# Kernel tuning notes

Measured on AMD Instinct MI355X. Metric: run time of the kernel, lower is better.

Reference implementation:

```python
import jax, jax.numpy as jnp
import numpy as np
from jax import lax


def _binarize(t):
    # sign binarization to +1/-1 (zero maps to -1, matching torch.where(t > 0, 1, -1))
    return jnp.where(t > 0, 1.0, -1.0).astype(t.dtype)


def _bconv(x, w, b):
    # binary conv: binarize input and weights, then standard 3x3 'same' conv
    y = lax.conv_general_dilated(
        _binarize(x), _binarize(w),
        window_strides=(1, 1), padding=((1, 1), (1, 1)),
        dimension_numbers=('NCHW', 'OIHW', 'NCHW'))
    return y + b[None, :, None, None]


def _maxpool2(x):
    return lax.reduce_window(x, -jnp.inf, lax.max, (1, 1, 2, 2), (1, 1, 2, 2), 'VALID')


def setup_inputs() -> dict:
    key = jax.random.key(0)
    ks = jax.random.split(key, 13)
    s = 0.1
    return {
        'x': jax.random.normal(ks[0], (4096, 1, 28, 28), jnp.float32),
        'w1': jax.random.normal(ks[1], (32, 1, 3, 3), jnp.float32) * s,
        'b1': jax.random.normal(ks[2], (32,), jnp.float32) * s,
        'w2': jax.random.normal(ks[3], (64, 32, 3, 3), jnp.float32) * s,
        'b2': jax.random.normal(ks[4], (64,), jnp.float32) * s,
        'w3': jax.random.normal(ks[5], (16, 64, 3, 3), jnp.float32) * s,
        'b3': jax.random.normal(ks[6], (16,), jnp.float32) * s,
        'fc1_w': jax.random.normal(ks[7], (256, 16 * 7 * 7), jnp.float32) * s,
        'fc1_b': jax.random.normal(ks[8], (256,), jnp.float32) * s,
        'fc2_w': jax.random.normal(ks[9], (128, 256), jnp.float32) * s,
        'fc2_b': jax.random.normal(ks[10], (128,), jnp.float32) * s,
        'fc3_w': jax.random.normal(ks[11], (10, 128), jnp.float32) * s,
        'fc3_b': jax.random.normal(ks[12], (10,), jnp.float32) * s,
    }


def reference(x, w1, b1, w2, b2, w3, b3, fc1_w, fc1_b, fc2_w, fc2_b, fc3_w, fc3_b):
    h = jax.nn.relu(_maxpool2(_bconv(x, w1, b1)))      # [B,32,14,14]
    h = jax.nn.relu(_maxpool2(_bconv(h, w2, b2)))      # [B,64,7,7]
    h = jax.nn.relu(_bconv(h, w3, b3))                 # [B,16,7,7]
    h = h.reshape(-1, 16 * 7 * 7)
    h = jax.nn.relu(h @ fc1_w.T + fc1_b)
    h = jax.nn.relu(h @ fc2_w.T + fc2_b)
    return h @ fc3_w.T + fc3_b                          # [B,10]
```

## Files before the change

### kernel.cpp

```cpp
#include <hip/hip_runtime.h>
#include <cstdint>

#define OFF_PW    0
#define OFF_W1T   4096
#define OFF_W2T   823296
#define OFF_H3T   954368
#define OFF_H1T   14061568
#define OFF_H2T   18255872

__global__ __launch_bounds__(256) void prep(
    const float* __restrict__ w1, const float* __restrict__ w2,
    const float* __restrict__ w3,
    const float* __restrict__ fc1_w, const float* __restrict__ fc2_w,
    uint32_t* __restrict__ pw, float* __restrict__ w1T, float* __restrict__ w2T) {
    int t = threadIdx.x;
    if (blockIdx.x == 0) {
        if (t < 32) {
            uint32_t b = 0;
            for (int k = 0; k < 9; ++k) b |= (w1[t * 9 + k] > 0.f ? 1u : 0u) << k;
            pw[t] = b;
        }
        for (int idx = t; idx < 576; idx += 256) {
            int oc = idx / 9, tap = idx % 9;
            int kh = tap / 3, kw = tap % 3;
            uint32_t b = 0;
            for (int ic = 0; ic < 32; ++ic)
                b |= (w2[((oc * 32 + ic) * 3 + kh) * 3 + kw] > 0.f ? 1u : 0u) << ic;
            pw[32 + idx] = b;
        }
        for (int idx = t; idx < 144; idx += 256) {
            int oc = idx / 9, tap = idx % 9;
            int kh = tap / 3, kw = tap % 3;
            uint32_t lo = 0, hi = 0;
            for (int ic = 0; ic < 32; ++ic) {
                lo |= (w3[((oc * 64 + ic) * 3 + kh) * 3 + kw] > 0.f ? 1u : 0u) << ic;
                hi |= (w3[((oc * 64 + ic + 32) * 3 + kh) * 3 + kw] > 0.f ? 1u : 0u) << ic;
            }
            pw[608 + idx * 2] = lo;
            pw[608 + idx * 2 + 1] = hi;
        }
    } else {
        int e = (blockIdx.x - 1) * 256 + t;
        if (e < 204800) {
            int k = e >> 8, n = e & 255;
            w1T[e] = (k < 784) ? fc1_w[n * 784 + k] : 0.f;
        } else {
            int e2 = e - 204800;
            int k = e2 >> 7, n = e2 & 127;
            w2T[e2] = fc2_w[n * 256 + k];
        }
    }
}

__global__ __launch_bounds__(256) void conv_stack(
    const float* __restrict__ x,
    const float* __restrict__ b1, const float* __restrict__ b2,
    const float* __restrict__ b3,
    const uint32_t* __restrict__ pw,
    float* __restrict__ h3T) {
    __shared__ uint32_t s_wb1[32];
    __shared__ uint32_t s_W2[576];
    __shared__ uint32_t s_W3[288];
    __shared__ float s_b1[32], s_b2[64], s_b3[16];
    __shared__ uint32_t s_xrow[28];
    __shared__ uint32_t s_H1[256];
    __shared__ uint32_t s_H2[162];

    const int t = threadIdx.x;
    const int img = blockIdx.x;

    s_H1[t] = 0;
    if (t < 162) s_H2[t] = 0;
    if (t < 32) { s_wb1[t] = pw[t]; s_b1[t] = b1[t]; }
    if (t >= 32 && t < 96) s_b2[t - 32] = b2[t - 32];
    if (t >= 96 && t < 112) s_b3[t - 96] = b3[t - 96];
    for (int i = t; i < 576; i += 256) s_W2[i] = pw[32 + i];
    for (int i = t; i < 288; i += 256) s_W3[i] = pw[608 + i];
    if (t >= 192 && t < 220) {
        int r = t - 192;
        const float* xr = x + img * 784 + r * 28;
        uint32_t b = 0;
        for (int j = 0; j < 28; ++j) b |= (xr[j] > 0.f ? 1u : 0u) << j;
        s_xrow[r] = b;
    }
    __syncthreads();

    if (t < 196) {
        int pi = t / 14, pj = t % 14;
        uint32_t sarr[4], marr[4];
        int pcm[4];
#pragma unroll
        for (int p = 0; p < 4; ++p) {
            int i = 2 * pi + (p >> 1), j = 2 * pj + (p & 1);
            uint32_t sb = 0, mb = 0;
            int bit = 0;
#pragma unroll
            for (int di = -1; di <= 1; ++di) {
                int y = i + di;
                bool rv = (unsigned)y < 28u;
                uint32_t row = rv ? s_xrow[rv ? y : 0] : 0u;
#pragma unroll
                for (int dj = -1; dj <= 1; ++dj) {
                    int xx = j + dj;
                    bool v = rv && (unsigned)xx < 28u;
                    if (v) {
                        mb |= 1u << bit;
                        sb |= ((row >> xx) & 1u) << bit;
                    }
                    ++bit;
                }
            }
            sarr[p] = sb; marr[p] = mb; pcm[p] = __popc(mb);
        }
        uint32_t word = 0;
#pragma unroll
        for (int c = 0; c < 32; ++c) {
            uint32_t w = s_wb1[c];
            int best = -1000;
#pragma unroll
            for (int p = 0; p < 4; ++p) {
                int v = pcm[p] - 2 * __popc((sarr[p] ^ w) & marr[p]);
                best = v > best ? v : best;
            }
            word |= ((float)best + s_b1[c] > 0.f ? 1u : 0u) << c;
        }
        s_H1[(pi + 1) * 16 + (pj + 1)] = word;
    }
    __syncthreads();

    for (int task = t; task < 400; task += 256) {
        int q = task / 25, ip = task - q * 25;
        int pi = ip / 5 + 1, pj = ip % 5 + 1;
        uint32_t cell[16];
#pragma unroll
        for (int r = 0; r < 4; ++r)
#pragma unroll
            for (int c = 0; c < 4; ++c)
                cell[r * 4 + c] = s_H1[(2 * pi + r) * 16 + (2 * pj + c)];
        uint32_t nib = 0;
#pragma unroll
        for (int o = 0; o < 4; ++o) {
            int oc = q * 4 + o;
            const uint32_t* wrow = &s_W2[oc * 9];
            int best = -100000;
#pragma unroll
            for (int a = 0; a < 2; ++a)
#pragma unroll
                for (int b = 0; b < 2; ++b) {
                    int S = 0;
#pragma unroll
                    for (int kh = 0; kh < 3; ++kh)
#pragma unroll
                        for (int kw = 0; kw < 3; ++kw)
                            S += __popc(cell[(a + kh) * 4 + (b + kw)] ^ wrow[kh * 3 + kw]);
                    int v = 288 - 2 * S;
                    best = v > best ? v : best;
                }
            nib |= ((float)best + s_b2[oc] > 0.f ? 1u : 0u) << (oc & 31);
        }
        atomicOr((unsigned int*)&s_H2[((pi + 1) * 9 + (pj + 1)) * 2 + (q >> 3)],
                 (unsigned int)nib);
    }
    for (int task = t; task < 384; task += 256) {
        int q = task / 24, bp = task - q * 24;
        int pi, pj;
        if (bp < 7)       { pi = 0; pj = bp; }
        else if (bp < 14) { pi = 6; pj = bp - 7; }
        else if (bp < 19) { pi = bp - 13; pj = 0; }
        else              { pi = bp - 18; pj = 6; }
        uint32_t vr[4], vc[4];
#pragma unroll
        for (int r = 0; r < 4; ++r) {
            vr[r] = ((unsigned)(2 * pi - 1 + r) < 14u) ? 0xFFFFFFFFu : 0u;
            vc[r] = ((unsigned)(2 * pj - 1 + r) < 14u) ? 0xFFFFFFFFu : 0u;
        }
        uint32_t cell[16], V[16];
#pragma unroll
        for (int r = 0; r < 4; ++r)
#pragma unroll
            for (int c = 0; c < 4; ++c) {
                cell[r * 4 + c] = s_H1[(2 * pi + r) * 16 + (2 * pj + c)];
                V[r * 4 + c] = vr[r] & vc[c];
            }
        int nvp[4];
#pragma unroll
        for (int a = 0; a < 2; ++a)
#pragma unroll
            for (int b = 0; b < 2; ++b) {
                int i = 2 * pi + a, j = 2 * pj + b;
                int vy = 3 - (i == 0) - (i == 13);
                int vx = 3 - (j == 0) - (j == 13);
                nvp[a * 2 + b] = 32 * vy * vx;
            }
        uint32_t nib = 0;
#pragma unroll
        for (int o = 0; o < 4; ++o) {
            int oc = q * 4 + o;
            const uint32_t* wrow = &s_W2[oc * 9];
            int best = -100000;
#pragma unroll
            for (int a = 0; a < 2; ++a)
#pragma unroll
                for (int b = 0; b < 2; ++b) {
                    int S = 0;
#pragma unroll
                    for (int kh = 0; kh < 3; ++kh)
#pragma unroll
                        for (int kw = 0; kw < 3; ++kw) {
                            int ci = (a + kh) * 4 + (b + kw);
                            S += __popc((cell[ci] ^ wrow[kh * 3 + kw]) & V[ci]);
                        }
                    int v = nvp[a * 2 + b] - 2 * S;
                    best = v > best ? v : best;
                }
            nib |= ((float)best + s_b2[oc] > 0.f ? 1u : 0u) << (oc & 31);
        }
        atomicOr((unsigned int*)&s_H2[((pi + 1) * 9 + (pj + 1)) * 2 + (q >> 3)],
                 (unsigned int)nib);
    }
    __syncthreads();

    for (int task = t; task < 784; task += 256) {
        int oc = task / 49, pos = task - oc * 49;
        int pi = pos / 7, pj = pos % 7;
        uint32_t vr[3], vc[3];
#pragma unroll
        for (int d = 0; d < 3; ++d) {
            vr[d] = ((unsigned)(pi - 1 + d) < 7u) ? 0xFFFFFFFFu : 0u;
            vc[d] = ((unsigned)(pj - 1 + d) < 7u) ? 0xFFFFFFFFu : 0u;
        }
        int vy = 3 - (pi == 0) - (pi == 6);
        int vx = 3 - (pj == 0) - (pj == 6);
        int Nv = 64 * vy * vx;
        const uint32_t* wr = &s_W3[oc * 18];
        int S = 0;
#pragma unroll
        for (int kh = 0; kh < 3; ++kh)
#pragma unroll
            for (int kw = 0; kw < 3; ++kw) {
                uint32_t V = vr[kh] & vc[kw];
                int idx = ((pi + kh) * 9 + (pj + kw)) * 2;
                S += __popc((s_H2[idx] ^ wr[(kh * 3 + kw) * 2]) & V);
                S += __popc((s_H2[idx + 1] ^ wr[(kh * 3 + kw) * 2 + 1]) & V);
            }
        float h = (float)(Nv - 2 * S) + s_b3[oc];
        h3T[task * 4096 + img] = h > 0.f ? h : 0.f;
    }
}

__global__ __launch_bounds__(256) void fc1_gemm(
    const float* __restrict__ aT,
    const float* __restrict__ bT,
    const float* __restrict__ bias,
    float* __restrict__ oT) {
    const int KC = 80, LD = 68;
    __shared__ float As[KC * LD];
    __shared__ float Bs[KC * LD];
    const int t = threadIdx.x;
    const int tx = t & 15, ty = t >> 4;
    const int img0 = blockIdx.x * 64;
    const int n0 = blockIdx.y * 64;
    float acc[4][4] = {{0.f}};

    for (int kc = 0; kc < 800; kc += KC) {
#pragma unroll
        for (int s = 0; s < 5; ++s) {
            int v = t + s * 256;
            int kk = v >> 4, i4 = (v & 15) * 4;
            *(float4*)&As[kk * LD + i4] =
                *(const float4*)&aT[(kc + kk) * 4096 + img0 + i4];
            *(float4*)&Bs[kk * LD + i4] =
                *(const float4*)&bT[(kc + kk) * 256 + n0 + i4];
        }
        __syncthreads();
#pragma unroll 4
        for (int kk = 0; kk < KC; ++kk) {
            float4 a = *(const float4*)&As[kk * LD + ty * 4];
            float4 b = *(const float4*)&Bs[kk * LD + tx * 4];
            acc[0][0] += a.x * b.x; acc[0][1] += a.x * b.y;
            acc[0][2] += a.x * b.z; acc[0][3] += a.x * b.w;
            acc[1][0] += a.y * b.x; acc[1][1] += a.y * b.y;
            acc[1][2] += a.y * b.z; acc[1][3] += a.y * b.w;
            acc[2][0] += a.z * b.x; acc[2][1] += a.z * b.y;
            acc[2][2] += a.z * b.z; acc[2][3] += a.z * b.w;
            acc[3][0] += a.w * b.x; acc[3][1] += a.w * b.y;
            acc[3][2] += a.w * b.z; acc[3][3] += a.w * b.w;
        }
        __syncthreads();
    }
    float4 bb = *(const float4*)&bias[n0 + tx * 4];
    float bv[4] = {bb.x, bb.y, bb.z, bb.w};
#pragma unroll
    for (int jj = 0; jj < 4; ++jj) {
        float4 ov;
        ov.x = acc[0][jj] + bv[jj]; ov.x = ov.x > 0.f ? ov.x : 0.f;
        ov.y = acc[1][jj] + bv[jj]; ov.y = ov.y > 0.f ? ov.y : 0.f;
        ov.z = acc[2][jj] + bv[jj]; ov.z = ov.z > 0.f ? ov.z : 0.f;
        ov.w = acc[3][jj] + bv[jj]; ov.w = ov.w > 0.f ? ov.w : 0.f;
        *(float4*)&oT[(n0 + tx * 4 + jj) * 4096 + img0 + ty * 4] = ov;
    }
}

__global__ __launch_bounds__(256) void fc2_gemm(
    const float* __restrict__ aT,
    const float* __restrict__ bT,
    const float* __restrict__ bias,
    float* __restrict__ oT) {
    const int KC = 64, LDA = 68, LDB = 36;
    __shared__ float As[KC * LDA];
    __shared__ float Bs[KC * LDB];
    const int t = threadIdx.x;
    const int tx = t & 15, ty = t >> 4;
    const int img0 = blockIdx.x * 64;
    const int n0 = blockIdx.y * 32;
    float acc[4][2] = {{0.f}};

    for (int kc = 0; kc < 256; kc += KC) {
#pragma unroll
        for (int s = 0; s < 4; ++s) {
            int v = t + s * 256;
            int kk = v >> 4, i4 = (v & 15) * 4;
            *(float4*)&As[kk * LDA + i4] =
                *(const float4*)&aT[(kc + kk) * 4096 + img0 + i4];
        }
#pragma unroll
        for (int s = 0; s < 2; ++s) {
            int v = t + s * 256;
            int kk = v >> 3, n4 = (v & 7) * 4;
            *(float4*)&Bs[kk * LDB + n4] =
                *(const float4*)&bT[(kc + kk) * 128 + n0 + n4];
        }
        __syncthreads();
#pragma unroll 4
        for (int kk = 0; kk < KC; ++kk) {
            float4 a = *(const float4*)&As[kk * LDA + ty * 4];
            float2 b = *(const float2*)&Bs[kk * LDB + tx * 2];
            acc[0][0] += a.x * b.x; acc[0][1] += a.x * b.y;
            acc[1][0] += a.y * b.x; acc[1][1] += a.y * b.y;
            acc[2][0] += a.z * b.x; acc[2][1] += a.z * b.y;
            acc[3][0] += a.w * b.x; acc[3][1] += a.w * b.y;
        }
        __syncthreads();
    }
#pragma unroll
    for (int j = 0; j < 2; ++j) {
        int n = n0 + tx * 2 + j;
        float bj = bias[n];
        float4 ov;
        ov.x = acc[0][j] + bj; ov.x = ov.x > 0.f ? ov.x : 0.f;
        ov.y = acc[1][j] + bj; ov.y = ov.y > 0.f ? ov.y : 0.f;
        ov.z = acc[2][j] + bj; ov.z = ov.z > 0.f ? ov.z : 0.f;
        ov.w = acc[3][j] + bj; ov.w = ov.w > 0.f ? ov.w : 0.f;
        *(float4*)&oT[n * 4096 + img0 + ty * 4] = ov;
    }
}

__global__ __launch_bounds__(256) void fc3_gemm(
    const float* __restrict__ aT,
    const float* __restrict__ w,
    const float* __restrict__ bias,
    float* __restrict__ out) {
    int id = blockIdx.x * 256 + threadIdx.x;
    int n = id >> 12, img = id & 4095;
    const float* wr = w + n * 128;
    float a0 = 0.f, a1 = 0.f, a2 = 0.f, a3 = 0.f;
#pragma unroll 8
    for (int k = 0; k < 128; k += 4) {
        a0 += aT[(k + 0) * 4096 + img] * wr[k + 0];
        a1 += aT[(k + 1) * 4096 + img] * wr[k + 1];
        a2 += aT[(k + 2) * 4096 + img] * wr[k + 2];
        a3 += aT[(k + 3) * 4096 + img] * wr[k + 3];
    }
    out[img * 10 + n] = (a0 + a1) + (a2 + a3) + bias[n];
}

extern "C" void kernel_launch(void* const* d_in, const int* in_sizes, int n_in,
                              void* d_out, int out_size, void* d_ws, size_t ws_size,
                              hipStream_t stream) {
    const float* x     = (const float*)d_in[0];
    const float* w1    = (const float*)d_in[1];
    const float* b1    = (const float*)d_in[2];
    const float* w2    = (const float*)d_in[3];
    const float* b2    = (const float*)d_in[4];
    const float* w3    = (const float*)d_in[5];
    const float* b3    = (const float*)d_in[6];
    const float* fc1_w = (const float*)d_in[7];
    const float* fc1_b = (const float*)d_in[8];
    const float* fc2_w = (const float*)d_in[9];
    const float* fc2_b = (const float*)d_in[10];
    const float* fc3_w = (const float*)d_in[11];
    const float* fc3_b = (const float*)d_in[12];
    float* out = (float*)d_out;

    const int B = in_sizes[0] / 784;
    char* ws = (char*)d_ws;
    uint32_t* pw = (uint32_t*)(ws + OFF_PW);
    float* w1T = (float*)(ws + OFF_W1T);
    float* w2T = (float*)(ws + OFF_W2T);
    float* h3T = (float*)(ws + OFF_H3T);
    float* h1T = (float*)(ws + OFF_H1T);
    float* h2T = (float*)(ws + OFF_H2T);

    hipLaunchKernelGGL(prep, dim3(929), dim3(256), 0, stream,
                       w1, w2, w3, fc1_w, fc2_w, pw, w1T, w2T);
    hipLaunchKernelGGL(conv_stack, dim3(B), dim3(256), 0, stream,
                       x, b1, b2, b3, pw, h3T);
    hipLaunchKernelGGL(fc1_gemm, dim3(B / 64, 4), dim3(256), 0, stream,
                       h3T, w1T, fc1_b, h1T);
    hipLaunchKernelGGL(fc2_gemm, dim3(B / 64, 4), dim3(256), 0, stream,
                       h1T, w2T, fc2_b, h2T);
    hipLaunchKernelGGL(fc3_gemm, dim3(B * 10 / 256), dim3(256), 0, stream,
                       h2T, fc3_w, fc3_b, out);
}
```

Before: 220.1 us.

## Rework binary conv stack with border corrections and double-buffered FC GEMMs

Rewrites the weight prep as a flat per-element kernel that packs sign bits with atomicOr, and zero-fills the padded rows of the fc1 activation buffer. The conv kernel now uses unmasked popcounts for interior pixels and precomputed border-correction tables for edges, compares against integer thresholds instead of float bias adds, and splits conv2/conv3 work by output-channel groups across threads. The fc1 and fc2 GEMMs gain register-staged double buffering in shared memory. These target ALU work in the conv stack and load latency in the GEMMs, at the cost of more complex indexing and an extra memset launch.

Result: slower. 250.5 us (+13.8%).

```diff
diff --git a/kernel.cpp b/kernel.cpp
--- a/kernel.cpp
+++ b/kernel.cpp
@@ -12,57 +12,64 @@
     const float* __restrict__ w1, const float* __restrict__ w2,
     const float* __restrict__ w3,
     const float* __restrict__ fc1_w, const float* __restrict__ fc2_w,
-    uint32_t* __restrict__ pw, float* __restrict__ w1T, float* __restrict__ w2T) {
-    int t = threadIdx.x;
-    if (blockIdx.x == 0) {
-        if (t < 32) {
-            uint32_t b = 0;
-            for (int k = 0; k < 9; ++k) b |= (w1[t * 9 + k] > 0.f ? 1u : 0u) << k;
-            pw[t] = b;
-        }
-        for (int idx = t; idx < 576; idx += 256) {
-            int oc = idx / 9, tap = idx % 9;
-            int kh = tap / 3, kw = tap % 3;
-            uint32_t b = 0;
-            for (int ic = 0; ic < 32; ++ic)
-                b |= (w2[((oc * 32 + ic) * 3 + kh) * 3 + kw] > 0.f ? 1u : 0u) << ic;
-            pw[32 + idx] = b;
-        }
-        for (int idx = t; idx < 144; idx += 256) {
-            int oc = idx / 9, tap = idx % 9;
-            int kh = tap / 3, kw = tap % 3;
-            uint32_t lo = 0, hi = 0;
-            for (int ic = 0; ic < 32; ++ic) {
-                lo |= (w3[((oc * 64 + ic) * 3 + kh) * 3 + kw] > 0.f ? 1u : 0u) << ic;
-                hi |= (w3[((oc * 64 + ic + 32) * 3 + kh) * 3 + kw] > 0.f ? 1u : 0u) << ic;
-            }
-            pw[608 + idx * 2] = lo;
-            pw[608 + idx * 2 + 1] = hi;
-        }
-    } else {
-        int e = (blockIdx.x - 1) * 256 + t;
-        if (e < 204800) {
-            int k = e >> 8, n = e & 255;
-            w1T[e] = (k < 784) ? fc1_w[n * 784 + k] : 0.f;
-        } else {
-            int e2 = e - 204800;
-            int k = e2 >> 7, n = e2 & 127;
-            w2T[e2] = fc2_w[n * 256 + k];
-        }
-    }
-}
-
-__global__ __launch_bounds__(256) void conv_stack(
-    const float* __restrict__ x,
-    const float* __restrict__ b1, const float* __restrict__ b2,
-    const float* __restrict__ b3,
-    const uint32_t* __restrict__ pw,
-    float* __restrict__ h3T) {
-    __shared__ uint32_t s_wb1[32];
-    __shared__ uint32_t s_W2[576];
+    uint32_t* __restrict__ pw, float* __restrict__ w1T,
+    float* __restrict__ w2T, float* __restrict__ h3T) {
+    int idx = blockIdx.x * 256 + threadIdx.x;
+    if (idx < 204800) {
+        int k = idx >> 8, n = idx & 255;
+        w1T[idx] = (k < 784) ? fc1_w[n * 784 + k] : 0.f;
+        return;
+    }
+    idx -= 204800;
+    if (idx < 32768) {
+        int k = idx >> 7, n = idx & 127;
+        w2T[idx] = fc2_w[n * 256 + k];
+        return;
+    }
+    idx -= 32768;
+    if (idx < 65536) {
+        h3T[784 * 4096 + idx] = 0.f;
+        return;
+    }
+    idx -= 65536;
+    if (idx < 288) {
+        int c = idx / 9, tap = idx - c * 9;
+        if (w1[idx] > 0.f) atomicOr(&pw[c], 1u << tap);
+        return;
+    }
+    idx -= 288;
+    if (idx < 18432) {
+        int oc = idx / 288, r = idx - oc * 288;
+        int ic = r / 9, tap = r - ic * 9;
+        if (w2[idx] > 0.f) atomicOr(&pw[32 + oc * 9 + tap], 1u << ic);
+        return;
+    }
+    idx -= 18432;
+    if (idx < 9216) {
+        int oc = idx / 576, r = idx - oc * 576;
+        int ic = r / 9, tap = r - ic * 9;
+        if (w3[idx] > 0.f)
+            atomicOr(&pw[608 + oc * 18 + tap * 2 + (ic >> 5)], 1u << (ic & 31));
+    }
+}
+
+__device__ __forceinline__ uint32_t bfe3(uint32_t r, int j) {
+    return (r >> j) & 7u;
+}
+
+__global__ __launch_bounds__(256, 4) void conv_stack(
+    const float* __restrict__ x, const float* __restrict__ b1,
+    const float* __restrict__ b2, const float* __restrict__ b3,
+    const uint32_t* __restrict__ pw, float* __restrict__ h3T) {
+    __shared__ uint32_t s_w1[32];
+    __shared__ int s_ic1[32];
+    __shared__ int s_ic2[64];
+    __shared__ uint32_t s_c2[128];
+    __shared__ uint32_t s_c3[32];
+    __shared__ uint32_t s_W2p[768];
     __shared__ uint32_t s_W3[288];
-    __shared__ float s_b1[32], s_b2[64], s_b3[16];
-    __shared__ uint32_t s_xrow[28];
+    __shared__ float s_b3[16];
+    __shared__ uint32_t s_xr[28];
     __shared__ uint32_t s_H1[256];
     __shared__ uint32_t s_H2[162];
 
@@ -71,212 +78,300 @@
 
     s_H1[t] = 0;
     if (t < 162) s_H2[t] = 0;
-    if (t < 32) { s_wb1[t] = pw[t]; s_b1[t] = b1[t]; }
-    if (t >= 32 && t < 96) s_b2[t - 32] = b2[t - 32];
-    if (t >= 96 && t < 112) s_b3[t - 96] = b3[t - 96];
-    for (int i = t; i < 576; i += 256) s_W2[i] = pw[32 + i];
+    if (t < 28) {
+        const float4* xr = (const float4*)(x + img * 784 + t * 28);
+        uint32_t b = 0;
+#pragma unroll
+        for (int q = 0; q < 7; ++q) {
+            float4 v = xr[q];
+            b |= (v.x > 0.f ? 1u : 0u) << (q * 4 + 0);
+            b |= (v.y > 0.f ? 1u : 0u) << (q * 4 + 1);
+            b |= (v.z > 0.f ? 1u : 0u) << (q * 4 + 2);
+            b |= (v.w > 0.f ? 1u : 0u) << (q * 4 + 3);
+        }
+        s_xr[t] = b << 1;
+    }
+    if (t >= 32 && t < 64) {
+        int c = t - 32;
+        s_w1[c] = pw[c];
+        s_ic1[c] = (int)floorf(-b1[c]) + 1;
+    }
+    if (t >= 64 && t < 128) {
+        int oc = t - 64;
+        s_ic2[oc] = (int)floorf(-b2[oc]) + 1;
+        int p[9];
+#pragma unroll
+        for (int k = 0; k < 9; ++k) p[k] = __popc(pw[32 + oc * 9 + k]);
+        s_c2[oc * 2] = (uint32_t)(p[0] + p[1] + p[2]) |
+                       ((uint32_t)(p[6] + p[7] + p[8]) << 8) |
+                       ((uint32_t)(p[0] + p[3] + p[6]) << 16) |
+                       ((uint32_t)(p[2] + p[5] + p[8]) << 24);
+        s_c2[oc * 2 + 1] = (uint32_t)p[0] | ((uint32_t)p[2] << 8) |
+                           ((uint32_t)p[6] << 16) | ((uint32_t)p[8] << 24);
+    }
+    if (t >= 128 && t < 144) {
+        int oc = t - 128;
+        s_b3[oc] = b3[oc];
+        int p[9];
+#pragma unroll
+        for (int k = 0; k < 9; ++k)
+            p[k] = __popc(pw[608 + oc * 18 + k * 2]) +
+                   __popc(pw[608 + oc * 18 + k * 2 + 1]);
+        s_c3[oc * 2] = (uint32_t)(p[0] + p[1] + p[2]) |
+                       ((uint32_t)(p[6] + p[7] + p[8]) << 8) |
+                       ((uint32_t)(p[0] + p[3] + p[6]) << 16) |
+                       ((uint32_t)(p[2] + p[5] + p[8]) << 24);
+        s_c3[oc * 2 + 1] = (uint32_t)p[0] | ((uint32_t)p[2] << 8) |
+                           ((uint32_t)p[6] << 16) | ((uint32_t)p[8] << 24);
+    }
+    for (int i = t; i < 768; i += 256) {
+        int oc = i / 12, tap = i - oc * 12;
+        s_W2p[i] = (tap < 9) ? pw[32 + oc * 9 + tap] : 0u;
+    }
     for (int i = t; i < 288; i += 256) s_W3[i] = pw[608 + i];
-    if (t >= 192 && t < 220) {
-        int r = t - 192;
-        const float* xr = x + img * 784 + r * 28;
-        uint32_t b = 0;
-        for (int j = 0; j < 28; ++j) b |= (xr[j] > 0.f ? 1u : 0u) << j;
-        s_xrow[r] = b;
-    }
     __syncthreads();
 
     if (t < 196) {
-        int pi = t / 14, pj = t % 14;
-        uint32_t sarr[4], marr[4];
-        int pcm[4];
-#pragma unroll
-        for (int p = 0; p < 4; ++p) {
-            int i = 2 * pi + (p >> 1), j = 2 * pj + (p & 1);
-            uint32_t sb = 0, mb = 0;
-            int bit = 0;
-#pragma unroll
-            for (int di = -1; di <= 1; ++di) {
-                int y = i + di;
-                bool rv = (unsigned)y < 28u;
-                uint32_t row = rv ? s_xrow[rv ? y : 0] : 0u;
-#pragma unroll
-                for (int dj = -1; dj <= 1; ++dj) {
-                    int xx = j + dj;
-                    bool v = rv && (unsigned)xx < 28u;
-                    if (v) {
-                        mb |= 1u << bit;
-                        sb |= ((row >> xx) & 1u) << bit;
-                    }
-                    ++bit;
+        int pi, pj;
+        if (t < 144) { pi = 1 + t / 12; pj = 1 + t % 12; }
+        else {
+            int b = t - 144;
+            if (b < 14)      { pi = 0;  pj = b; }
+            else if (b < 28) { pi = 13; pj = b - 14; }
+            else if (b < 40) { pi = 1 + (b - 28); pj = 0; }
+            else             { pi = 1 + (b - 40); pj = 13; }
+        }
+        uint32_t r[4];
+#pragma unroll
+        for (int k = 0; k < 4; ++k) {
+            int y = 2 * pi - 1 + k;
+            r[k] = ((unsigned)y < 28u) ? s_xr[y] : 0u;
+        }
+        uint32_t samp[4];
+#pragma unroll
+        for (int a = 0; a < 2; ++a)
+#pragma unroll
+            for (int bb = 0; bb < 2; ++bb) {
+                int j = 2 * pj + bb;
+                samp[a * 2 + bb] = bfe3(r[a], j) | (bfe3(r[a + 1], j) << 3) |
+                                   (bfe3(r[a + 2], j) << 6);
+            }
+        uint32_t word = 0;
+        if (t < 144) {
+#pragma unroll 4
+            for (int c = 0; c < 32; ++c) {
+                uint32_t w = s_w1[c];
+                int S = __popc(samp[0] ^ w);
+                int S1 = __popc(samp[1] ^ w); S = S1 < S ? S1 : S;
+                int S2 = __popc(samp[2] ^ w); S = S2 < S ? S2 : S;
+                int S3 = __popc(samp[3] ^ w); S = S3 < S ? S3 : S;
+                word |= (uint32_t)(9 - 2 * S >= s_ic1[c]) << c;
+            }
+        } else {
+            uint32_t inv[4];
+            int Nv[4];
+#pragma unroll
+            for (int a = 0; a < 2; ++a)
+#pragma unroll
+                for (int bb = 0; bb < 2; ++bb) {
+                    int i = 2 * pi + a, j = 2 * pj + bb;
+                    inv[a * 2 + bb] =
+                        (i == 0 ? 0x7u : 0u) | (i == 27 ? 0x1C0u : 0u) |
+                        (j == 0 ? 0x49u : 0u) | (j == 27 ? 0x124u : 0u);
                 }
-            }
-            sarr[p] = sb; marr[p] = mb; pcm[p] = __popc(mb);
-        }
-        uint32_t word = 0;
-#pragma unroll
-        for (int c = 0; c < 32; ++c) {
-            uint32_t w = s_wb1[c];
-            int best = -1000;
-#pragma unroll
-            for (int p = 0; p < 4; ++p) {
-                int v = pcm[p] - 2 * __popc((sarr[p] ^ w) & marr[p]);
-                best = v > best ? v : best;
-            }
-            word |= ((float)best + s_b1[c] > 0.f ? 1u : 0u) << c;
-        }
-        s_H1[(pi + 1) * 16 + (pj + 1)] = word;
+#pragma unroll
+            for (int p = 0; p < 4; ++p) Nv[p] = 9 - __popc(inv[p]);
+#pragma unroll 4
+            for (int c = 0; c < 32; ++c) {
+                uint32_t w = s_w1[c];
+                int vmax = -100;
+#pragma unroll
+                for (int p = 0; p < 4; ++p) {
+                    int v = Nv[p] - 2 * (__popc(samp[p] ^ w) - __popc(w & inv[p]));
+                    vmax = v > vmax ? v : vmax;
+                }
+                word |= (uint32_t)(vmax >= s_ic1[c]) << c;
+            }
+        }
+        s_H1[(pi + 1) * 16 + pj + 1] = word;
     }
     __syncthreads();
 
-    for (int task = t; task < 400; task += 256) {
-        int q = task / 25, ip = task - q * 25;
-        int pi = ip / 5 + 1, pj = ip % 5 + 1;
+    if (t < 245) {
+        int pos = t / 5, grp = t - pos * 5;
+        int pi, pj;
+        if (pos < 25) { pi = 1 + pos / 5; pj = 1 + pos % 5; }
+        else {
+            int b = pos - 25;
+            if (b < 7)       { pi = 0; pj = b; }
+            else if (b < 14) { pi = 6; pj = b - 7; }
+            else if (b < 19) { pi = b - 13; pj = 0; }
+            else             { pi = b - 18; pj = 6; }
+        }
         uint32_t cell[16];
 #pragma unroll
         for (int r = 0; r < 4; ++r)
 #pragma unroll
             for (int c = 0; c < 4; ++c)
                 cell[r * 4 + c] = s_H1[(2 * pi + r) * 16 + (2 * pj + c)];
-        uint32_t nib = 0;
+        const bool border = pos >= 25;
+        int rsh = (pi == 6) ? 8 : 0;
+        uint32_t mR = (pi == 0) ? 0x3u : ((pi == 6) ? 0xCu : 0u);
+        int csh = (pj == 6) ? 24 : 16;
+        uint32_t mC = (pj == 0) ? 0x5u : ((pj == 6) ? 0xAu : 0u);
+        int pcell = ((pi == 6) ? 2 : 0) + ((pj == 6) ? 1 : 0);
+        int psh = pcell * 8;
+        uint32_t mP = (mR && mC) ? (1u << pcell) : 0u;
+        int Nv[4];
+#pragma unroll
+        for (int p = 0; p < 4; ++p) {
+            int rP = (mR >> p) & 1, cP = (mC >> p) & 1;
+            Nv[p] = 32 * (9 - 3 * rP - 3 * cP + (rP & cP));
+        }
+        int ocs = grp * 13;
+        int cnt = (grp < 4) ? 13 : 12;
+        uint32_t lo = 0, hi = 0;
+        for (int oi = 0; oi < cnt; ++oi) {
+            int oc = ocs + oi;
+            const uint32_t* wp = &s_W2p[oc * 12];
+            uint4 wA = *(const uint4*)wp;
+            uint4 wB = *(const uint4*)(wp + 4);
+            uint32_t w8 = wp[8];
+            uint32_t w[9] = {wA.x, wA.y, wA.z, wA.w, wB.x, wB.y, wB.z, wB.w, w8};
+            int S[4];
+#pragma unroll
+            for (int a = 0; a < 2; ++a)
+#pragma unroll
+                for (int bb = 0; bb < 2; ++bb) {
+                    int acc = 0;
+#pragma unroll
+                    for (int kh = 0; kh < 3; ++kh)
+#pragma unroll
+                        for (int kw = 0; kw < 3; ++kw)
+                            acc += __popc(cell[(a + kh) * 4 + (bb + kw)] ^ w[kh * 3 + kw]);
+                    S[a * 2 + bb] = acc;
+                }
+            int bitv;
+            if (!border) {
+                int Sm = S[0];
+                Sm = S[1] < Sm ? S[1] : Sm;
+                Sm = S[2] < Sm ? S[2] : Sm;
+                Sm = S[3] < Sm ? S[3] : Sm;
+                bitv = (288 - 2 * Sm >= s_ic2[oc]) ? 1 : 0;
+            } else {
+                uint32_t cw0 = s_c2[oc * 2], cw1 = s_c2[oc * 2 + 1];
+                int rB = (cw0 >> rsh) & 0xFF;
+                int cB = (cw0 >> csh) & 0xFF;
+                int pB = (cw1 >> psh) & 0xFF;
+                int vmax = -100000;
+#pragma unroll
+                for (int p = 0; p < 4; ++p) {
+                    int corr = (((mR >> p) & 1) ? rB : 0) +
+                               (((mC >> p) & 1) ? cB : 0) -
+                               (((mP >> p) & 1) ? pB : 0);
+                    int v = Nv[p] - 2 * (S[p] - corr);
+                    vmax = v > vmax ? v : vmax;
+                }
+                bitv = (vmax >= s_ic2[oc]) ? 1 : 0;
+            }
+            if (oc < 32) lo |= (uint32_t)bitv << oc;
+            else         hi |= (uint32_t)bitv << (oc - 32);
+        }
+        int hidx = ((pi + 1) * 9 + pj + 1) * 2;
+        if (lo) atomicOr(&s_H2[hidx], lo);
+        if (hi) atomicOr(&s_H2[hidx + 1], hi);
+    }
+    __syncthreads();
+
+    if (t < 196) {
+        int pos = t >> 2, grp = t & 3;
+        int pi, pj;
+        if (pos < 25) { pi = 1 + pos / 5; pj = 1 + pos % 5; }
+        else {
+            int b = pos - 25;
+            if (b < 7)       { pi = 0; pj = b; }
+            else if (b < 14) { pi = 6; pj = b - 7; }
+            else if (b < 19) { pi = b - 13; pj = 0; }
+            else             { pi = b - 18; pj = 6; }
+        }
+        uint32_t cc[18];
+#pragma unroll
+        for (int kh = 0; kh < 3; ++kh)
+#pragma unroll
+            for (int kw = 0; kw < 3; ++kw) {
+                int bidx = ((pi + kh) * 9 + pj + kw) * 2;
+                cc[(kh * 3 + kw) * 2] = s_H2[bidx];
+                cc[(kh * 3 + kw) * 2 + 1] = s_H2[bidx + 1];
+            }
+        const bool border = pos >= 25;
+        int rowAny = (pi == 0) | (pi == 6);
+        int colAny = (pj == 0) | (pj == 6);
+        int rsh = (pi == 6) ? 8 : 0;
+        int csh = (pj == 6) ? 24 : 16;
+        int psh = (((pi == 6) ? 2 : 0) + ((pj == 6) ? 1 : 0)) * 8;
+        int nInv = 3 * rowAny + 3 * colAny - (rowAny & colAny);
+        int NvB = 64 * (9 - nInv);
 #pragma unroll
         for (int o = 0; o < 4; ++o) {
-            int oc = q * 4 + o;
-            const uint32_t* wrow = &s_W2[oc * 9];
-            int best = -100000;
-#pragma unroll
-            for (int a = 0; a < 2; ++a)
-#pragma unroll
-                for (int b = 0; b < 2; ++b) {
-                    int S = 0;
-#pragma unroll
-                    for (int kh = 0; kh < 3; ++kh)
-#pragma unroll
-                        for (int kw = 0; kw < 3; ++kw)
-                            S += __popc(cell[(a + kh) * 4 + (b + kw)] ^ wrow[kh * 3 + kw]);
-                    int v = 288 - 2 * S;
-                    best = v > best ? v : best;
-                }
-            nib |= ((float)best + s_b2[oc] > 0.f ? 1u : 0u) << (oc & 31);
-        }
-        atomicOr((unsigned int*)&s_H2[((pi + 1) * 9 + (pj + 1)) * 2 + (q >> 3)],
-                 (unsigned int)nib);
-    }
-    for (int task = t; task < 384; task += 256) {
-        int q = task / 24, bp = task - q * 24;
-        int pi, pj;
-        if (bp < 7)       { pi = 0; pj = bp; }
-        else if (bp < 14) { pi = 6; pj = bp - 7; }
-        else if (bp < 19) { pi = bp - 13; pj = 0; }
-        else              { pi = bp - 18; pj = 6; }
-        uint32_t vr[4], vc[4];
-#pragma unroll
-        for (int r = 0; r < 4; ++r) {
-            vr[r] = ((unsigned)(2 * pi - 1 + r) < 14u) ? 0xFFFFFFFFu : 0u;
-            vc[r] = ((unsigned)(2 * pj - 1 + r) < 14u) ? 0xFFFFFFFFu : 0u;
-        }
-        uint32_t cell[16], V[16];
-#pragma unroll
-        for (int r = 0; r < 4; ++r)
-#pragma unroll
-            for (int c = 0; c < 4; ++c) {
-                cell[r * 4 + c] = s_H1[(2 * pi + r) * 16 + (2 * pj + c)];
-                V[r * 4 + c] = vr[r] & vc[c];
-            }
-        int nvp[4];
-#pragma unroll
-        for (int a = 0; a < 2; ++a)
-#pragma unroll
-            for (int b = 0; b < 2; ++b) {
-                int i = 2 * pi + a, j = 2 * pj + b;
-                int vy = 3 - (i == 0) - (i == 13);
-                int vx = 3 - (j == 0) - (j == 13);
-                nvp[a * 2 + b] = 32 * vy * vx;
-            }
-        uint32_t nib = 0;
-#pragma unroll
-        for (int o = 0; o < 4; ++o) {
-            int oc = q * 4 + o;
-            const uint32_t* wrow = &s_W2[oc * 9];
-            int best = -100000;
-#pragma unroll
-            for (int a = 0; a < 2; ++a)
-#pragma unroll
-                for (int b = 0; b < 2; ++b) {
-                    int S = 0;
-#pragma unroll
-                    for (int kh = 0; kh < 3; ++kh)
-#pragma unroll
-                        for (int kw = 0; kw < 3; ++kw) {
-                            int ci = (a + kh) * 4 + (b + kw);
-                            S += __popc((cell[ci] ^ wrow[kh * 3 + kw]) & V[ci]);
-                        }
-                    int v = nvp[a * 2 + b] - 2 * S;
-                    best = v > best ? v : best;
-                }
-            nib |= ((float)best + s_b2[oc] > 0.f ? 1u : 0u) << (oc & 31);
-        }
-        atomicOr((unsigned int*)&s_H2[((pi + 1) * 9 + (pj + 1)) * 2 + (q >> 3)],
-                 (unsigned int)nib);
-    }
-    __syncthreads();
-
-    for (int task = t; task < 784; task += 256) {
-        int oc = task / 49, pos = task - oc * 49;
-        int pi = pos / 7, pj = pos % 7;
-        uint32_t vr[3], vc[3];
-#pragma unroll
-        for (int d = 0; d < 3; ++d) {
-            vr[d] = ((unsigned)(pi - 1 + d) < 7u) ? 0xFFFFFFFFu : 0u;
-            vc[d] = ((unsigned)(pj - 1 + d) < 7u) ? 0xFFFFFFFFu : 0u;
-        }
-        int vy = 3 - (pi == 0) - (pi == 6);
-        int vx = 3 - (pj == 0) - (pj == 6);
-        int Nv = 64 * vy * vx;
-        const uint32_t* wr = &s_W3[oc * 18];
-        int S = 0;
-#pragma unroll
-        for (int kh = 0; kh < 3; ++kh)
-#pragma unroll
-            for (int kw = 0; kw < 3; ++kw) {
-                uint32_t V = vr[kh] & vc[kw];
-                int idx = ((pi + kh) * 9 + (pj + kw)) * 2;
-                S += __popc((s_H2[idx] ^ wr[(kh * 3 + kw) * 2]) & V);
-                S += __popc((s_H2[idx + 1] ^ wr[(kh * 3 + kw) * 2 + 1]) & V);
-            }
-        float h = (float)(Nv - 2 * S) + s_b3[oc];
-        h3T[task * 4096 + img] = h > 0.f ? h : 0.f;
-    }
-}
-
-__global__ __launch_bounds__(256) void fc1_gemm(
-    const float* __restrict__ aT,
-    const float* __restrict__ bT,
-    const float* __restrict__ bias,
-    float* __restrict__ oT) {
-    const int KC = 80, LD = 68;
-    __shared__ float As[KC * LD];
-    __shared__ float Bs[KC * LD];
+            int oc = grp * 4 + o;
+            const uint32_t* wp = &s_W3[oc * 18];
+            int S = 0;
+#pragma unroll
+            for (int k = 0; k < 18; ++k) S += __popc(cc[k] ^ wp[k]);
+            int corr = 0;
+            if (border) {
+                uint32_t cw0 = s_c3[oc * 2], cw1 = s_c3[oc * 2 + 1];
+                corr = (rowAny ? (int)((cw0 >> rsh) & 0xFF) : 0) +
+                       (colAny ? (int)((cw0 >> csh) & 0xFF) : 0) -
+                       ((rowAny & colAny) ? (int)((cw1 >> psh) & 0xFF) : 0);
+            }
+            int v = NvB - 2 * (S - corr);
+            float h = (float)v + s_b3[oc];
+            h3T[(oc * 49 + pi * 7 + pj) * 4096 + img] = fmaxf(h, 0.f);
+        }
+    }
+}
+
+__global__ __launch_bounds__(256, 1) void fc1_gemm(
+    const float* __restrict__ aT, const float* __restrict__ bT,
+    const float* __restrict__ bias, float* __restrict__ oT) {
+    __shared__ float As[2][50 * 68];
+    __shared__ float Bs[2][50 * 68];
     const int t = threadIdx.x;
     const int tx = t & 15, ty = t >> 4;
     const int img0 = blockIdx.x * 64;
     const int n0 = blockIdx.y * 64;
     float acc[4][4] = {{0.f}};
 
-    for (int kc = 0; kc < 800; kc += KC) {
-#pragma unroll
-        for (int s = 0; s < 5; ++s) {
-            int v = t + s * 256;
+#pragma unroll
+    for (int s = 0; s < 4; ++s) {
+        int v = t + s * 256;
+        if (v < 800) {
             int kk = v >> 4, i4 = (v & 15) * 4;
-            *(float4*)&As[kk * LD + i4] =
-                *(const float4*)&aT[(kc + kk) * 4096 + img0 + i4];
-            *(float4*)&Bs[kk * LD + i4] =
-                *(const float4*)&bT[(kc + kk) * 256 + n0 + i4];
-        }
-        __syncthreads();
-#pragma unroll 4
-        for (int kk = 0; kk < KC; ++kk) {
-            float4 a = *(const float4*)&As[kk * LD + ty * 4];
-            float4 b = *(const float4*)&Bs[kk * LD + tx * 4];
+            *(float4*)&As[0][kk * 68 + i4] = *(const float4*)&aT[kk * 4096 + img0 + i4];
+            *(float4*)&Bs[0][kk * 68 + i4] = *(const float4*)&bT[kk * 256 + n0 + i4];
+        }
+    }
+    __syncthreads();
+    int cur = 0;
+    for (int ch = 0; ch < 16; ++ch) {
+        float4 ra[4], rb[4];
+        if (ch < 15) {
+            int kc = (ch + 1) * 50;
+#pragma unroll
+            for (int s = 0; s < 4; ++s) {
+                int v = t + s * 256;
+                if (v < 800) {
+                    int kk = v >> 4, i4 = (v & 15) * 4;
+                    ra[s] = *(const float4*)&aT[(kc + kk) * 4096 + img0 + i4];
+                    rb[s] = *(const float4*)&bT[(kc + kk) * 256 + n0 + i4];
+                }
+            }
+        }
+#pragma unroll 5
+        for (int kk = 0; kk < 50; ++kk) {
+            float4 a = *(const float4*)&As[cur][kk * 68 + ty * 4];
+            float4 b = *(const float4*)&Bs[cur][kk * 68 + tx * 4];
             acc[0][0] += a.x * b.x; acc[0][1] += a.x * b.y;
             acc[0][2] += a.x * b.z; acc[0][3] += a.x * b.w;
             acc[1][0] += a.y * b.x; acc[1][1] += a.y * b.y;
@@ -286,7 +381,19 @@
             acc[3][0] += a.w * b.x; acc[3][1] += a.w * b.y;
             acc[3][2] += a.w * b.z; acc[3][3] += a.w * b.w;
         }
+        if (ch < 15) {
+#pragma unroll
+            for (int s = 0; s < 4; ++s) {
+                int v = t + s * 256;
+                if (v < 800) {
+                    int kk = v >> 4, i4 = (v & 15) * 4;
+                    *(float4*)&As[cur ^ 1][kk * 68 + i4] = ra[s];
+                    *(float4*)&Bs[cur ^ 1][kk * 68 + i4] = rb[s];
+                }
+            }
+        }
         __syncthreads();
+        cur ^= 1;
     }
     float4 bb = *(const float4*)&bias[n0 + tx * 4];
     float bv[4] = {bb.x, bb.y, bb.z, bb.w};
@@ -301,46 +408,73 @@
     }
 }
 
-__global__ __launch_bounds__(256) void fc2_gemm(
-    const float* __restrict__ aT,
-    const float* __restrict__ bT,
-    const float* __restrict__ bias,
-    float* __restrict__ oT) {
-    const int KC = 64, LDA = 68, LDB = 36;
-    __shared__ float As[KC * LDA];
-    __shared__ float Bs[KC * LDB];
+__global__ __launch_bounds__(256, 1) void fc2_gemm(
+    const float* __restrict__ aT, const float* __restrict__ bT,
+    const float* __restrict__ bias, float* __restrict__ oT) {
+    __shared__ float As[2][64 * 68];
+    __shared__ float Bs[2][64 * 36];
     const int t = threadIdx.x;
     const int tx = t & 15, ty = t >> 4;
     const int img0 = blockIdx.x * 64;
     const int n0 = blockIdx.y * 32;
     float acc[4][2] = {{0.f}};
 
-    for (int kc = 0; kc < 256; kc += KC) {
-#pragma unroll
-        for (int s = 0; s < 4; ++s) {
-            int v = t + s * 256;
-            int kk = v >> 4, i4 = (v & 15) * 4;
-            *(float4*)&As[kk * LDA + i4] =
-                *(const float4*)&aT[(kc + kk) * 4096 + img0 + i4];
-        }
-#pragma unroll
-        for (int s = 0; s < 2; ++s) {
-            int v = t + s * 256;
-            int kk = v >> 3, n4 = (v & 7) * 4;
-            *(float4*)&Bs[kk * LDB + n4] =
-                *(const float4*)&bT[(kc + kk) * 128 + n0 + n4];
-        }
-        __syncthreads();
+#pragma unroll
+    for (int s = 0; s < 4; ++s) {
+        int v = t + s * 256;
+        int kk = v >> 4, i4 = (v & 15) * 4;
+        *(float4*)&As[0][kk * 68 + i4] = *(const float4*)&aT[kk * 4096 + img0 + i4];
+    }
+#pragma unroll
+    for (int s = 0; s < 2; ++s) {
+        int v = t + s * 256;
+        int kk = v >> 3, n4 = (v & 7) * 4;
+        *(float4*)&Bs[0][kk * 36 + n4] = *(const float4*)&bT[kk * 128 + n0 + n4];
+    }
+    __syncthreads();
+    int cur = 0;
+    for (int ch = 0; ch < 4; ++ch) {
+        float4 ra[4]; float4 rb[2];
+        if (ch < 3) {
+            int kc = (ch + 1) * 64;
+#pragma unroll
+            for (int s = 0; s < 4; ++s) {
+                int v = t + s * 256;
+                int kk = v >> 4, i4 = (v & 15) * 4;
+                ra[s] = *(const float4*)&aT[(kc + kk) * 4096 + img0 + i4];
+            }
+#pragma unroll
+            for (int s = 0; s < 2; ++s) {
+                int v = t + s * 256;
+                int kk = v >> 3, n4 = (v & 7) * 4;
+                rb[s] = *(const float4*)&bT[(kc + kk) * 128 + n0 + n4];
+            }
+        }
 #pragma unroll 4
-        for (int kk = 0; kk < KC; ++kk) {
-            float4 a = *(const float4*)&As[kk * LDA + ty * 4];
-            float2 b = *(const float2*)&Bs[kk * LDB + tx * 2];
+        for (int kk = 0; kk < 64; ++kk) {
+            float4 a = *(const float4*)&As[cur][kk * 68 + ty * 4];
+            float2 b = *(const float2*)&Bs[cur][kk * 36 + tx * 2];
             acc[0][0] += a.x * b.x; acc[0][1] += a.x * b.y;
             acc[1][0] += a.y * b.x; acc[1][1] += a.y * b.y;
             acc[2][0] += a.z * b.x; acc[2][1] += a.z * b.y;
             acc[3][0] += a.w * b.x; acc[3][1] += a.w * b.y;
         }
+        if (ch < 3) {
+#pragma unroll
+            for (int s = 0; s < 4; ++s) {
+                int v = t + s * 256;
+                int kk = v >> 4, i4 = (v & 15) * 4;
+                *(float4*)&As[cur ^ 1][kk * 68 + i4] = ra[s];
+            }
+#pragma unroll
+            for (int s = 0; s < 2; ++s) {
+                int v = t + s * 256;
+                int kk = v >> 3, n4 = (v & 7) * 4;
+                *(float4*)&Bs[cur ^ 1][kk * 36 + n4] = rb[s];
+            }
+        }
         __syncthreads();
+        cur ^= 1;
     }
 #pragma unroll
     for (int j = 0; j < 2; ++j) {
@@ -356,10 +490,8 @@
 }
 
 __global__ __launch_bounds__(256) void fc3_gemm(
-    const float* __restrict__ aT,
-    const float* __restrict__ w,
-    const float* __restrict__ bias,
-    float* __restrict__ out) {
+    const float* __restrict__ aT, const float* __restrict__ w,
+    const float* __restrict__ bias, float* __restrict__ out) {
     int id = blockIdx.x * 256 + threadIdx.x;
     int n = id >> 12, img = id & 4095;
     const float* wr = w + n * 128;
@@ -401,8 +533,9 @@
     float* h1T = (float*)(ws + OFF_H1T);
     float* h2T = (float*)(ws + OFF_H2T);
 
-    hipLaunchKernelGGL(prep, dim3(929), dim3(256), 0, stream,
-                       w1, w2, w3, fc1_w, fc2_w, pw, w1T, w2T);
+    hipMemsetAsync(pw, 0, 896 * 4, stream);
+    hipLaunchKernelGGL(prep, dim3(1294), dim3(256), 0, stream,
+                       w1, w2, w3, fc1_w, fc2_w, pw, w1T, w2T, h3T);
     hipLaunchKernelGGL(conv_stack, dim3(B), dim3(256), 0, stream,
                        x, b1, b2, b3, pw, h3T);
     hipLaunchKernelGGL(fc1_gemm, dim3(B / 64, 4), dim3(256), 0, stream,
```
